# Kernel optimization log

Measured on AMD Instinct MI355X. Metric: run time of the kernel, lower is better.

The kernel has to match this reference:

```python
import jax, jax.numpy as jnp
import numpy as np

NUM_CAPS = 2          # NUM_CLASSES
R = 16 * 10 * 10 * 10 # num_route_nodes = 16000
NUM_ITERS = 3


def conv3d(x, w, b, stride):
    y = jax.lax.conv_general_dilated(
        x, w, window_strides=(stride, stride, stride), padding='VALID',
        dimension_numbers=('NCDHW', 'OIDHW', 'NCDHW'))
    return y + b[None, :, None, None, None]


def squash(t, axis=-1):
    n = jnp.linalg.norm(t, axis=axis, keepdims=True)
    scale = n ** 2 / (1 + n ** 2) / (n + 1e-8)
    return scale * t


def setup_inputs() -> dict:
    key = jax.random.key(0)
    ks = jax.random.split(key, 16)
    inp = {
        'x': jax.random.normal(ks[0], (16, 1, 29, 29, 29), jnp.float32),
        'conv1_w': 0.05 * jax.random.normal(ks[1], (128, 1, 3, 3, 3), jnp.float32),
        'conv1_b': jnp.zeros((128,), jnp.float32),
        # 8 primary capsules, each Conv3d(128,16,k=9,s=2), stacked cap-major
        'pcaps_w': 0.01 * jax.random.normal(ks[2], (8 * 16, 128, 9, 9, 9), jnp.float32),
        'pcaps_b': jnp.zeros((8 * 16,), jnp.float32),
        'route_w': 0.01 * jax.random.normal(ks[3], (NUM_CAPS, R, 8, 16), jnp.float32),
        'dec_w1': 0.05 * jax.random.normal(ks[4], (32, 512), jnp.float32),
        'dec_b1': jnp.zeros((512,), jnp.float32),
        'dec_w2': 0.05 * jax.random.normal(ks[5], (512, 2048), jnp.float32),
        'dec_b2': jnp.zeros((2048,), jnp.float32),
        'dec_w3': 0.02 * jax.random.normal(ks[6], (2048, 10240), jnp.float32),
        'dec_b3': jnp.zeros((10240,), jnp.float32),
        'dec_w4': 0.02 * jax.random.normal(ks[7], (10240, 27000), jnp.float32),
        'dec_b4': jnp.zeros((27000,), jnp.float32),
    }
    return inp


def reference(x, conv1_w, conv1_b, pcaps_w, pcaps_b, route_w,
              dec_w1, dec_b1, dec_w2, dec_b2, dec_w3, dec_b3, dec_w4, dec_b4):
    B = x.shape[0]
    # stem conv + relu: [B,128,27,27,27]
    h = jax.nn.relu(conv3d(x, conv1_w, conv1_b, 1))
    # primary capsules (8 convs fused into one): [B,128,10,10,10]
    p = conv3d(h, pcaps_w, pcaps_b, 2)
    # torch: per-capsule view(B,-1,1) then cat dim=-1 -> [B,16000,8]
    p = p.reshape(B, 8, R).transpose(0, 2, 1)
    u = squash(p, axis=-1)  # [B,R,8]

    # priors: x[:,None,:,None,:] @ W[None] -> [B,C,R,16] (singleton dim dropped)
    priors = jnp.einsum('bri,crio->bcro', u, route_w)
    priors_d = jax.lax.stop_gradient(priors)
    # torch logits have trailing dim 16 but are constant along it (delta is
    # broadcast), so [B,C,R,1] is mathematically identical.
    logits = jnp.zeros((B, NUM_CAPS, R, 1), priors.dtype)

    for i in range(NUM_ITERS):
        probs = jax.nn.softmax(logits, axis=1)  # over capsule axis
        if i == NUM_ITERS - 1:
            v = squash((probs * priors).sum(axis=2, keepdims=True))
        else:
            v = squash((probs * priors_d).sum(axis=2, keepdims=True))
            logits = logits + (priors_d * v).sum(axis=-1, keepdims=True)

    caps = v[:, :, 0, :]  # [B,C,16] (squeeze)
    classes = jnp.linalg.norm(caps, axis=-1)  # [B,C]

    # y=None branch: one-hot of argmax
    y = jax.nn.one_hot(jnp.argmax(classes, axis=1), NUM_CAPS, dtype=caps.dtype)
    d = (caps * y[:, :, None]).reshape(B, -1)  # [B,32]
    d = jax.nn.relu(d @ dec_w1 + dec_b1)
    d = jax.nn.relu(d @ dec_w2 + dec_b2)
    d = jax.nn.relu(d @ dec_w3 + dec_b3)
    recon = jax.nn.sigmoid(d @ dec_w4 + dec_b4)  # [B,27000]
    return classes, recon
```

## Files before the change

kernel.cpp:

```cpp
#include <hip/hip_runtime.h>
#include <hip/hip_bf16.h>

#define NB   16
#define C1   128
#define XS   29
#define HS   27
#define HSP  19683
#define PS   10
#define PSP  1000
#define RR   16000
#define NCAP 2
#define KTAP 729
#define HTOT 40310784L
#define SPTOT 314928

#define OFF_WT   0UL
#define OFF_H    11943936UL
#define OFF_P    52254720UL
#define OFF_U    54302720UL
#define OFF_PRI  56350720UL
#define OFF_LOG  64542720UL
#define OFF_S    65054720UL
#define OFF_V    65055232UL
#define OFF_D0   65055744UL
#define OFF_D1   65056256UL
#define OFF_D2   65064448UL
#define OFF_D3   65097216UL
#define OFF_D4   65261056UL
#define OFF_PP   65693056UL
#define OFF_D3P  82077056UL
#define OFF_D4P  84698496UL

typedef __attribute__((ext_vector_type(8))) short bf16x8;
typedef __attribute__((ext_vector_type(4))) float f32x4;

#define GL2LDS16(g, l) __builtin_amdgcn_global_load_lds( \
    (const __attribute__((address_space(1))) void*)(g), \
    (__attribute__((address_space(3))) void*)(l), 16, 0, 0)

__global__ void prep_w2(const float* __restrict__ w, __hip_bfloat16* __restrict__ w2) {
    __shared__ float tile[32][33];
    int tap0 = blockIdx.x * 32;
    int ic0  = blockIdx.y * 32;
    int oc   = blockIdx.z;
    int tx = threadIdx.x & 31, ty = threadIdx.x >> 5;
    #pragma unroll
    for (int j = 0; j < 32; j += 8) {
        int tap = tap0 + tx, ic = ic0 + ty + j;
        if (tap < KTAP) tile[ty + j][tx] = w[(size_t)oc * 93312 + (size_t)ic * KTAP + tap];
    }
    __syncthreads();
    #pragma unroll
    for (int j = 0; j < 32; j += 8) {
        int tap = tap0 + ty + j, ic = ic0 + tx;
        if (tap < KTAP)
            w2[((size_t)tap * 128 + oc) * 128 + ic] = __float2bfloat16(tile[tx][ty + j]);
    }
}

__global__ __launch_bounds__(256) void conv1_relu(const float* __restrict__ x,
                                                  const float* __restrict__ w,
                                                  const float* __restrict__ bias,
                                                  __hip_bfloat16* __restrict__ h) {
    int t = threadIdx.x;
    int c = t & 127;
    float wr[27];
    #pragma unroll
    for (int k = 0; k < 27; k++) wr[k] = w[c * 27 + k];
    float bv = bias[c];
    int sp_base = blockIdx.x * 32 + (t >> 7);
    #pragma unroll 4
    for (int i = 0; i < 16; i++) {
        int spg = sp_base + i * 2;
        if (spg >= SPTOT) return;
        int b = spg / HSP, sp = spg % HSP;
        int z = sp / 729, y = (sp / 27) % 27, xx = sp % 27;
        const float* xb = x + (size_t)b * (XS * XS * XS) + ((size_t)z * XS + y) * XS + xx;
        float xv[27];
        #pragma unroll
        for (int dz = 0; dz < 3; dz++)
            #pragma unroll
            for (int dy = 0; dy < 3; dy++)
                #pragma unroll
                for (int dx = 0; dx < 3; dx++)
                    xv[(dz * 3 + dy) * 3 + dx] = xb[((size_t)dz * XS + dy) * XS + dx];
        float acc = bv;
        #pragma unroll
        for (int k = 0; k < 27; k++) acc = fmaf(xv[k], wr[k], acc);
        h[(size_t)spg * 128 + c] = __float2bfloat16(fmaxf(acc, 0.f));
    }
}

__global__ __launch_bounds__(512) void pcaps_mfma(const ushort* __restrict__ hu,
                                                  const ushort* __restrict__ wu,
                                                  float* __restrict__ pp) {
    __shared__ __align__(16) ushort As[256 * 64];
    __shared__ __align__(16) ushort Bs[128 * 64];
    int t = threadIdx.x;
    int bid = blockIdx.x;
    int g = bid & 7;
    int mtile = bid >> 3;
    int m0 = mtile * 256;
    int tap_begin = g * 92;
    int tap_end   = min(KTAP, tap_begin + 92);

    int arow[4];
    #pragma unroll
    for (int q = 0; q < 4; q++) {
        int idx = q * 512 + t;
        int row = idx >> 3, seg = idx & 7;
        int m = m0 + row; if (m > 15999) m = 15999;
        int b = m / PSP, sp = m % PSP;
        int oz = sp / 100, oy = (sp / 10) % 10, ox = sp % 10;
        arow[q] = (((b * HS + 2 * oz) * HS + 2 * oy) * HS + 2 * ox) * 128 + seg * 8;
    }
    int brow[2];
    #pragma unroll
    for (int q = 0; q < 2; q++) {
        int idx = q * 512 + t;
        brow[q] = (idx >> 3) * 128 + (idx & 7) * 8;
    }

    int lane = t & 63, wave = t >> 6;
    int wr = wave >> 1, wc = wave & 1;
    int l15 = lane & 15, kq = lane >> 4;

    f32x4 acc[4][4];
    #pragma unroll
    for (int i = 0; i < 4; i++)
        #pragma unroll
        for (int j = 0; j < 4; j++) acc[i][j] = (f32x4)0.f;

    for (int tap = tap_begin; tap < tap_end; ++tap) {
        int dz = tap / 81, dy = (tap / 9) % 9, dx = tap % 9;
        int tapoff = ((dz * HS + dy) * HS + dx) * 128;
        const ushort* wtap = wu + ((size_t)tap << 14);
        #pragma unroll
        for (int ich = 0; ich < 2; ++ich) {
            #pragma unroll
            for (int q = 0; q < 4; q++)
                GL2LDS16(hu + arow[q] + tapoff + ich * 64, As + ((size_t)(q * 512 + t)) * 8);
            #pragma unroll
            for (int q = 0; q < 2; q++)
                GL2LDS16(wtap + brow[q] + ich * 64, Bs + ((size_t)(q * 512 + t)) * 8);
            __syncthreads();
            #pragma unroll
            for (int ks = 0; ks < 2; ++ks) {
                bf16x8 av[4], bv[4];
                #pragma unroll
                for (int i = 0; i < 4; i++)
                    av[i] = *(const bf16x8*)&As[(wr * 64 + i * 16 + l15) * 64 + ks * 32 + kq * 8];
                #pragma unroll
                for (int j = 0; j < 4; j++)
                    bv[j] = *(const bf16x8*)&Bs[(wc * 64 + j * 16 + l15) * 64 + ks * 32 + kq * 8];
                #pragma unroll
                for (int i = 0; i < 4; i++)
                    #pragma unroll
                    for (int j = 0; j < 4; j++)
                        acc[i][j] = __builtin_amdgcn_mfma_f32_16x16x32_bf16(av[i], bv[j], acc[i][j], 0, 0, 0);
            }
            __syncthreads();
        }
    }

    float* pg = pp + (size_t)g * 16000 * 128;
    #pragma unroll
    for (int i = 0; i < 4; i++) {
        int mbase = m0 + wr * 64 + i * 16 + kq * 4;
        #pragma unroll
        for (int j = 0; j < 4; j++) {
            int n = wc * 64 + j * 16 + l15;
            #pragma unroll
            for (int r = 0; r < 4; r++) {
                int m = mbase + r;
                if (m < 16000) pg[(size_t)m * 128 + n] = acc[i][j][r];
            }
        }
    }
}

__global__ void reduce_p(const float* __restrict__ pp, float* __restrict__ p) {
    int gid = blockIdx.x * 256 + threadIdx.x;
    const float4* p4 = (const float4*)pp;
    float4 a = p4[gid];
    #pragma unroll
    for (int k = 1; k < 8; k++) {
        float4 b = p4[(size_t)k * 512000 + gid];
        a.x += b.x; a.y += b.y; a.z += b.z; a.w += b.w;
    }
    ((float4*)p)[gid] = a;
}

__global__ void squash_u(const float* __restrict__ p, const float* __restrict__ pb,
                         float* __restrict__ u) {
    int gid = blockIdx.x * 256 + threadIdx.x;
    int b = gid / RR, r = gid % RR;
    int s = r % PSP, rq = r / PSP;
    float vals[8]; float ss = 0.f;
    #pragma unroll
    for (int i = 0; i < 8; i++) {
        int ch = i * 16 + rq;
        float pv = p[((size_t)b * PSP + s) * 128 + ch] + pb[ch];
        vals[i] = pv; ss += pv * pv;
    }
    float n = sqrtf(ss);
    float scale = ss / (1.f + ss) / (n + 1e-8f);
    #pragma unroll
    for (int i = 0; i < 8; i++) u[(size_t)gid * 8 + i] = vals[i] * scale;
}

__global__ void priors_k(const float* __restrict__ u, const float* __restrict__ rw,
                         float* __restrict__ pri) {
    __shared__ float wl[16][132];
    int bx = blockIdx.x; int c = bx / 1000; int r0 = (bx % 1000) * 16;
    int t = threadIdx.x;
    const float4* src = (const float4*)(rw + ((size_t)c * RR + r0) * 128);
    #pragma unroll
    for (int q = 0; q < 8; q++) {
        int idx = q * 256 + t;
        int row = idx >> 5, c4 = idx & 31;
        *(float4*)&wl[row][c4 * 4] = src[idx];
    }
    __syncthreads();
    int bb = t >> 4, rl = t & 15;
    const float* up = u + ((size_t)bb * RR + r0 + rl) * 8;
    float4 u0 = *(const float4*)up, u1 = *(const float4*)(up + 4);
    float uu[8] = {u0.x, u0.y, u0.z, u0.w, u1.x, u1.y, u1.z, u1.w};
    float out[16];
    #pragma unroll
    for (int o = 0; o < 16; o++) out[o] = 0.f;
    #pragma unroll
    for (int i = 0; i < 8; i++)
        #pragma unroll
        for (int o = 0; o < 16; o++) out[o] += uu[i] * wl[rl][i * 16 + o];
    float* dst = pri + ((size_t)(bb * 2 + c) * RR + r0 + rl) * 16;
    #pragma unroll
    for (int q = 0; q < 4; q++)
        *(float4*)&dst[q * 4] = make_float4(out[q*4], out[q*4+1], out[q*4+2], out[q*4+3]);
}

__global__ void route_s(const float* __restrict__ pri, const float* __restrict__ lg,
                        float* __restrict__ s) {
    int b = blockIdx.x, chunk = blockIdx.y;
    int t = threadIdx.x, o = t & 15, rl = t >> 4;
    float acc0 = 0.f, acc1 = 0.f;
    for (int j = 0; j < 40; j++) {
        int r = chunk * 640 + j * 16 + rl;
        float l0 = lg[(size_t)(b * 2 + 0) * RR + r];
        float l1 = lg[(size_t)(b * 2 + 1) * RR + r];
        float m = fmaxf(l0, l1);
        float e0 = __expf(l0 - m), e1 = __expf(l1 - m);
        float inv = 1.f / (e0 + e1);
        acc0 += (e0 * inv) * pri[((size_t)(b * 2 + 0) * RR + r) * 16 + o];
        acc1 += (e1 * inv) * pri[((size_t)(b * 2 + 1) * RR + r) * 16 + o];
    }
    __shared__ float red[2][16][17];
    red[0][rl][o] = acc0; red[1][rl][o] = acc1;
    __syncthreads();
    for (int step = 8; step >= 1; step >>= 1) {
        if (rl < step) {
            red[0][rl][o] += red[0][rl + step][o];
            red[1][rl][o] += red[1][rl + step][o];
        }
        __syncthreads();
    }
    if (rl == 0) {
        atomicAdd(&s[(b * 2 + 0) * 16 + o], red[0][0][o]);
        atomicAdd(&s[(b * 2 + 1) * 16 + o], red[1][0][o]);
    }
}

__global__ void squash_v(const float* __restrict__ s, float* __restrict__ v) {
    int t = threadIdx.x;
    int bc = t >> 4, o = t & 15;
    float ss = 0.f;
    #pragma unroll
    for (int i = 0; i < 16; i++) { float x = s[bc * 16 + i]; ss += x * x; }
    float n = sqrtf(ss);
    float sc = ss / (1.f + ss) / (n + 1e-8f);
    v[bc * 16 + o] = s[bc * 16 + o] * sc;
}

__global__ void route_logit(const float* __restrict__ pri, const float* __restrict__ v,
                            float* __restrict__ lg) {
    int gid = blockIdx.x * 256 + threadIdx.x;
    int bc = gid / RR;
    const float* pp = pri + (size_t)gid * 16;
    float dot = 0.f;
    #pragma unroll
    for (int o = 0; o < 16; o++) dot += pp[o] * v[bc * 16 + o];
    lg[gid] += dot;
}

__global__ void classes_mask(const float* __restrict__ v, float* __restrict__ out,
                             float* __restrict__ d0) {
    __shared__ float cls[32];
    int t = threadIdx.x;
    if (t < 32) {
        float ss = 0.f;
        #pragma unroll
        for (int i = 0; i < 16; i++) { float x = v[t * 16 + i]; ss += x * x; }
        float n = sqrtf(ss);
        cls[t] = n; out[t] = n;
    }
    __syncthreads();
    int b = t >> 5, k = t & 31, c = k >> 4;
    int win = (cls[b * 2 + 1] > cls[b * 2 + 0]) ? 1 : 0;
    d0[t] = (c == win) ? v[b * 32 + k] : 0.f;
}

template<int K>
__global__ void dec_small(const float* __restrict__ din, const float* __restrict__ W,
                          const float* __restrict__ bias, float* __restrict__ dout, int N) {
    __shared__ float dl[16 * K];
    int t = threadIdx.x;
    for (int i = t; i < 16 * K; i += 256) dl[i] = din[i];
    __syncthreads();
    int n = blockIdx.x * 256 + t;
    if (n >= N) return;
    float acc[16];
    float bv = bias[n];
    #pragma unroll
    for (int b = 0; b < 16; b++) acc[b] = bv;
    for (int k = 0; k < K; k++) {
        float w = W[(size_t)k * N + n];
        #pragma unroll
        for (int b = 0; b < 16; b++) acc[b] += dl[b * K + k] * w;
    }
    #pragma unroll
    for (int b = 0; b < 16; b++) dout[(size_t)b * N + n] = fmaxf(acc[b], 0.f);
}

__global__ void dec_split(const float* __restrict__ din, const float* __restrict__ W,
                          float* __restrict__ part, int N, int K, int KC) {
    extern __shared__ float dl[];
    int t = threadIdx.x;
    int ky = blockIdx.y;
    int k0 = ky * KC;
    for (int i = t; i < 16 * KC; i += 256) {
        int b = i / KC, kk = i % KC;
        dl[i] = din[(size_t)b * K + k0 + kk];
    }
    __syncthreads();
    int n = blockIdx.x * 1024 + t * 4;
    if (n >= N) return;
    float4 acc[16];
    #pragma unroll
    for (int b = 0; b < 16; b++) acc[b] = make_float4(0.f, 0.f, 0.f, 0.f);
    const float* Wp = W + (size_t)k0 * N + n;
    for (int kk = 0; kk < KC; kk++) {
        float4 w = *(const float4*)&Wp[(size_t)kk * N];
        #pragma unroll
        for (int b = 0; b < 16; b++) {
            float dv = dl[b * KC + kk];
            acc[b].x += dv * w.x; acc[b].y += dv * w.y;
            acc[b].z += dv * w.z; acc[b].w += dv * w.w;
        }
    }
    #pragma unroll
    for (int b = 0; b < 16; b++)
        *(float4*)&part[((size_t)(ky * 16 + b)) * N + n] = acc[b];
}

__global__ void bias_act_sum(const float* __restrict__ part, const float* __restrict__ bias,
                             float* __restrict__ out, int N, int total, int sigm) {
    int gid = blockIdx.x * 256 + threadIdx.x;
    if (gid >= total) return;
    int b = gid / N, n = gid % N;
    float x = bias[n];
    #pragma unroll
    for (int ky = 0; ky < 16; ky++)
        x += part[((size_t)(ky * 16 + b)) * N + n];
    out[gid] = sigm ? (1.f / (1.f + __expf(-x))) : fmaxf(x, 0.f);
}

extern "C" void kernel_launch(void* const* d_in, const int* in_sizes, int n_in,
                              void* d_out, int out_size, void* d_ws, size_t ws_size,
                              hipStream_t stream) {
    const float* x        = (const float*)d_in[0];
    const float* conv1_w  = (const float*)d_in[1];
    const float* conv1_b  = (const float*)d_in[2];
    const float* pcaps_w  = (const float*)d_in[3];
    const float* pcaps_b  = (const float*)d_in[4];
    const float* route_w  = (const float*)d_in[5];
    const float* dec_w1   = (const float*)d_in[6];
    const float* dec_b1   = (const float*)d_in[7];
    const float* dec_w2   = (const float*)d_in[8];
    const float* dec_b2   = (const float*)d_in[9];
    const float* dec_w3   = (const float*)d_in[10];
    const float* dec_b3   = (const float*)d_in[11];
    const float* dec_w4   = (const float*)d_in[12];
    const float* dec_b4   = (const float*)d_in[13];
    float* out = (float*)d_out;

    float* ws = (float*)d_ws;
    __hip_bfloat16* w2 = (__hip_bfloat16*)(ws + OFF_WT);
    __hip_bfloat16* h  = (__hip_bfloat16*)(ws + OFF_H);
    float* p    = ws + OFF_P;
    float* u    = ws + OFF_U;
    float* pri  = ws + OFF_PRI;
    float* lg   = ws + OFF_LOG;
    float* s    = ws + OFF_S;
    float* v    = ws + OFF_V;
    float* d0   = ws + OFF_D0;
    float* d1   = ws + OFF_D1;
    float* d2   = ws + OFF_D2;
    float* d3   = ws + OFF_D3;
    float* d4   = ws + OFF_D4;
    float* pp   = ws + OFF_PP;
    float* d3p  = ws + OFF_D3P;
    float* d4p  = ws + OFF_D4P;

    prep_w2<<<dim3(23, 4, 128), 256, 0, stream>>>(pcaps_w, w2);
    conv1_relu<<<(SPTOT + 31) / 32, 256, 0, stream>>>(x, conv1_w, conv1_b, h);

    pcaps_mfma<<<504, 512, 0, stream>>>((const ushort*)h, (const ushort*)w2, pp);
    reduce_p<<<2000, 256, 0, stream>>>(pp, p);

    squash_u<<<1000, 256, 0, stream>>>(p, pcaps_b, u);
    priors_k<<<2000, 256, 0, stream>>>(u, route_w, pri);

    hipMemsetAsync(lg, 0, (size_t)NB * NCAP * RR * sizeof(float), stream);
    for (int it = 0; it < 3; it++) {
        hipMemsetAsync(s, 0, 512 * sizeof(float), stream);
        route_s<<<dim3(16, 25), 256, 0, stream>>>(pri, lg, s);
        squash_v<<<1, 512, 0, stream>>>(s, v);
        if (it < 2) route_logit<<<2000, 256, 0, stream>>>(pri, v, lg);
    }

    classes_mask<<<1, 512, 0, stream>>>(v, out, d0);

    dec_small<32><<<2, 256, 0, stream>>>(d0, dec_w1, dec_b1, d1, 512);
    dec_small<512><<<8, 256, 0, stream>>>(d1, dec_w2, dec_b2, d2, 2048);

    dec_split<<<dim3(10, 16), 256, 16 * 128 * sizeof(float), stream>>>(d2, dec_w3, d3p, 10240, 2048, 128);
    bias_act_sum<<<(16 * 10240 + 255) / 256, 256, 0, stream>>>(d3p, dec_b3, d3, 10240, 16 * 10240, 0);

    dec_split<<<dim3(27, 16), 256, 16 * 640 * sizeof(float), stream>>>(d3, dec_w4, d4p, 27000, 10240, 640);
    bias_act_sum<<<(16 * 27000 + 255) / 256, 256, 0, stream>>>(d4p, dec_b4, out + 32, 27000, 16 * 27000, 1);
}
```

Measured before the change: 1.214 ms.

## Double-buffer pcaps MFMA LDS tiles with swizzled layout and finer K steps

Restructures the primary-capsule implicit-GEMM loop to use two LDS buffers with K-chunks of 32, prefetching the next chunk via global-to-LDS loads while MFMAs consume the current one. LDS rows are XOR-swizzled to reduce bank conflicts, and launch bounds request two blocks per CU since LDS usage halves. The intent is to hide global load latency and improve occupancy. The cost is more barriers per unit of work, and the hand-written vmcnt wait could be fragile.

```diff
diff --git a/kernel.cpp b/kernel.cpp
--- a/kernel.cpp
+++ b/kernel.cpp
@@ -91,39 +91,37 @@
     }
 }
 
-__global__ __launch_bounds__(512) void pcaps_mfma(const ushort* __restrict__ hu,
-                                                  const ushort* __restrict__ wu,
-                                                  float* __restrict__ pp) {
-    __shared__ __align__(16) ushort As[256 * 64];
-    __shared__ __align__(16) ushort Bs[128 * 64];
+__global__ __launch_bounds__(512, 2) void pcaps_mfma(const ushort* __restrict__ hu,
+                                                     const ushort* __restrict__ wu,
+                                                     float* __restrict__ pp) {
+    __shared__ __align__(16) ushort As[2 * 256 * 32];
+    __shared__ __align__(16) ushort Bs[2 * 128 * 32];
     int t = threadIdx.x;
     int bid = blockIdx.x;
     int g = bid & 7;
-    int mtile = bid >> 3;
-    int m0 = mtile * 256;
+    int m0 = (bid >> 3) * 256;
     int tap_begin = g * 92;
     int tap_end   = min(KTAP, tap_begin + 92);
-
-    int arow[4];
-    #pragma unroll
-    for (int q = 0; q < 4; q++) {
+    int KP = (tap_end - tap_begin) * 4;
+
+    int a_base[2], a_seg[2];
+    #pragma unroll
+    for (int q = 0; q < 2; q++) {
         int idx = q * 512 + t;
-        int row = idx >> 3, seg = idx & 7;
+        int row = idx >> 2;
         int m = m0 + row; if (m > 15999) m = 15999;
         int b = m / PSP, sp = m % PSP;
         int oz = sp / 100, oy = (sp / 10) % 10, ox = sp % 10;
-        arow[q] = (((b * HS + 2 * oz) * HS + 2 * oy) * HS + 2 * ox) * 128 + seg * 8;
-    }
-    int brow[2];
-    #pragma unroll
-    for (int q = 0; q < 2; q++) {
-        int idx = q * 512 + t;
-        brow[q] = (idx >> 3) * 128 + (idx & 7) * 8;
-    }
+        a_base[q] = (((b * HS + 2 * oz) * HS + 2 * oy) * HS + 2 * ox) * 128;
+        a_seg[q]  = (((idx & 3) ^ ((idx >> 3) & 3))) * 8;
+    }
+    int b_base = (t >> 2) * 128;
+    int b_seg  = (((t & 3) ^ ((t >> 3) & 3))) * 8;
 
     int lane = t & 63, wave = t >> 6;
     int wr = wave >> 1, wc = wave & 1;
     int l15 = lane & 15, kq = lane >> 4;
+    int slot8 = (kq ^ ((l15 >> 1) & 3)) * 8;
 
     f32x4 acc[4][4];
     #pragma unroll
@@ -131,37 +129,43 @@
         #pragma unroll
         for (int j = 0; j < 4; j++) acc[i][j] = (f32x4)0.f;
 
-    for (int tap = tap_begin; tap < tap_end; ++tap) {
-        int dz = tap / 81, dy = (tap / 9) % 9, dx = tap % 9;
-        int tapoff = ((dz * HS + dy) * HS + dx) * 128;
-        const ushort* wtap = wu + ((size_t)tap << 14);
-        #pragma unroll
-        for (int ich = 0; ich < 2; ++ich) {
+#define STAGE(KPI, NB_)  {                                                   \
+        int tap_ = tap_begin + ((KPI) >> 2), ich_ = ((KPI) & 3) * 32;        \
+        int dz_ = tap_ / 81, dy_ = (tap_ / 9) % 9, dx_ = tap_ % 9;           \
+        int toff_ = ((dz_ * HS + dy_) * HS + dx_) * 128 + ich_;              \
+        const ushort* wt_ = wu + ((size_t)tap_ << 14) + ich_;                \
+        ushort* ad_ = As + (NB_) * (256 * 32);                               \
+        ushort* bd_ = Bs + (NB_) * (128 * 32);                               \
+        GL2LDS16(hu + a_base[0] + toff_ + a_seg[0], ad_ + (size_t)t * 8);    \
+        GL2LDS16(hu + a_base[1] + toff_ + a_seg[1], ad_ + (size_t)(512 + t) * 8); \
+        GL2LDS16(wt_ + b_base + b_seg, bd_ + (size_t)t * 8);                 \
+    }
+
+    STAGE(0, 0);
+    int cur = 0;
+    for (int kp = 0; kp < KP; ++kp) {
+        int nk = (kp + 1 < KP) ? kp + 1 : kp;
+        STAGE(nk, cur ^ 1);
+        asm volatile("s_waitcnt vmcnt(3)" ::: "memory");
+        __builtin_amdgcn_s_barrier();
+        const ushort* Ac = As + cur * (256 * 32);
+        const ushort* Bc = Bs + cur * (128 * 32);
+        bf16x8 av[4], bv[4];
+        #pragma unroll
+        for (int i = 0; i < 4; i++)
+            av[i] = *(const bf16x8*)&Ac[(wr * 64 + i * 16 + l15) * 32 + slot8];
+        #pragma unroll
+        for (int j = 0; j < 4; j++)
+            bv[j] = *(const bf16x8*)&Bc[(wc * 64 + j * 16 + l15) * 32 + slot8];
+        #pragma unroll
+        for (int i = 0; i < 4; i++)
             #pragma unroll
-            for (int q = 0; q < 4; q++)
-                GL2LDS16(hu + arow[q] + tapoff + ich * 64, As + ((size_t)(q * 512 + t)) * 8);
-            #pragma unroll
-            for (int q = 0; q < 2; q++)
-                GL2LDS16(wtap + brow[q] + ich * 64, Bs + ((size_t)(q * 512 + t)) * 8);
-            __syncthreads();
-            #pragma unroll
-            for (int ks = 0; ks < 2; ++ks) {
-                bf16x8 av[4], bv[4];
-                #pragma unroll
-                for (int i = 0; i < 4; i++)
-                    av[i] = *(const bf16x8*)&As[(wr * 64 + i * 16 + l15) * 64 + ks * 32 + kq * 8];
-                #pragma unroll
-                for (int j = 0; j < 4; j++)
-                    bv[j] = *(const bf16x8*)&Bs[(wc * 64 + j * 16 + l15) * 64 + ks * 32 + kq * 8];
-                #pragma unroll
-                for (int i = 0; i < 4; i++)
-                    #pragma unroll
-                    for (int j = 0; j < 4; j++)
-                        acc[i][j] = __builtin_amdgcn_mfma_f32_16x16x32_bf16(av[i], bv[j], acc[i][j], 0, 0, 0);
-            }
-            __syncthreads();
-        }
-    }
+            for (int j = 0; j < 4; j++)
+                acc[i][j] = __builtin_amdgcn_mfma_f32_16x16x32_bf16(av[i], bv[j], acc[i][j], 0, 0, 0);
+        __builtin_amdgcn_s_barrier();
+        cur ^= 1;
+    }
+#undef STAGE
 
     float* pg = pp + (size_t)g * 16000 * 128;
     #pragma unroll
```

Result: no change. 1.233 ms (+1.6%).
